# Kernel tuning notes

Hardware: AMD Instinct MI355X
Metric: run time of the kernel (lower is better)

## Reference

```python
import jax, jax.numpy as jnp
import numpy as np

N_NODES = 100000
N_EDGES = 3200000
N_FEAT = 128
HIDDEN = 16
MLP_H = 100
N_CLASSES = 12
N_GRAPHS = 512


def setup_inputs() -> dict:
    key = jax.random.key(0)
    ks = jax.random.split(key, 12)
    x = jax.random.normal(ks[0], (N_NODES, N_FEAT), dtype=jnp.float32)
    edge_index = jax.random.randint(ks[1], (2, N_EDGES), 0, N_NODES, dtype=jnp.int64)
    batch_vec = jnp.sort(jax.random.randint(ks[2], (N_NODES,), 0, N_GRAPHS, dtype=jnp.int64))
    def glorot(k, shape):
        lim = np.sqrt(6.0 / (shape[0] + shape[1]))
        return jax.random.uniform(k, shape, jnp.float32, -lim, lim)
    W1 = glorot(ks[3], (N_FEAT, HIDDEN)); b1 = jnp.zeros((HIDDEN,), jnp.float32)
    W2 = glorot(ks[4], (HIDDEN, HIDDEN)); b2 = jnp.zeros((HIDDEN,), jnp.float32)
    lw1 = glorot(ks[5], (HIDDEN, MLP_H)); lb1 = jnp.zeros((MLP_H,), jnp.float32)
    lw2 = glorot(ks[6], (MLP_H, N_CLASSES)); lb2 = jnp.zeros((N_CLASSES,), jnp.float32)
    return {"x": x, "edge_index": edge_index, "batch_vec": batch_vec,
            "W1": W1, "b1": b1, "W2": W2, "b2": b2,
            "lw1": lw1, "lb1": lb1, "lw2": lw2, "lb2": lb2}


def _gcn_edges(edge_index):
    # add self loops, compute symmetric normalization (PyG GCNConv default)
    loop = jnp.arange(N_NODES, dtype=edge_index.dtype)
    src = jnp.concatenate([edge_index[0], loop])
    dst = jnp.concatenate([edge_index[1], loop])
    deg = jax.ops.segment_sum(jnp.ones_like(dst, dtype=jnp.float32), dst,
                              num_segments=N_NODES)
    dinv = jnp.where(deg > 0, jax.lax.rsqrt(deg), 0.0)
    norm = dinv[src] * dinv[dst]  # [E+N]
    return src, dst, norm


def _gcn_conv(x, W, b, src, dst, norm):
    h = x @ W                                # [N, out]
    msg = h[src] * norm[:, None]             # gather + scale, [E+N, out]
    out = jax.ops.segment_sum(msg, dst, num_segments=N_NODES)
    return out + b


def reference(x, edge_index, batch_vec, W1, b1, W2, b2, lw1, lb1, lw2, lb2):
    src, dst, norm = _gcn_edges(edge_index)
    h = jax.nn.relu(_gcn_conv(x, W1, b1, src, dst, norm))   # dropout: eval no-op
    h = _gcn_conv(h, W2, b2, src, dst, norm)
    h = jax.nn.relu(h)
    pooled = jax.ops.segment_sum(h, batch_vec, num_segments=N_GRAPHS)  # global_add_pool
    g = jax.nn.relu(pooled)
    g = jax.nn.relu(g @ lw1 + lb1)
    return g @ lw2 + lb2  # [N_GRAPHS, N_CLASSES] logits
```

## Files before the change

### kernel.cpp

```cpp
#include <hip/hip_runtime.h>

#define N_NODES   100000
#define N_EDGES   3200000
#define N_FEAT    128
#define HIDDEN    16
#define MLP_H     100
#define N_CLASSES 12
#define N_GRAPHS  512
#define BNODES    512
#define NBUCK     196
#define BCAP      17328
#define CPAD      16
#define RING      64
#define BIN_BLOCKS 256
#define GEMM_BLOCKS 391

__global__ __launch_bounds__(256) void kInit(int* __restrict__ gcursor,
                                             float* __restrict__ pooled) {
    int t = blockIdx.x * 256 + threadIdx.x;
    if (t < NBUCK) gcursor[t * CPAD] = t * BCAP;
    if (t < N_GRAPHS * HIDDEN) pooled[t] = 0.f;
}

__global__ __launch_bounds__(256) void kBinGemm(const int* __restrict__ src,
                                                const int* __restrict__ dst,
                                                int* __restrict__ gcursor,
                                                int* __restrict__ pairs,
                                                const float* __restrict__ x,
                                                const float* __restrict__ W1,
                                                float* __restrict__ hp) {
    __shared__ union {
        struct { int ring[NBUCK * RING]; int cnt[NBUCK]; int fl[NBUCK]; } bin;
        float gw[N_FEAT * HIDDEN];
    } sm;
    int t = threadIdx.x;
    if (blockIdx.x < BIN_BLOCKS) {
        for (int i = t; i < NBUCK; i += 256) { sm.bin.cnt[i] = 0; sm.bin.fl[i] = 0; }
        __syncthreads();
        const int batch = 256 * 4;
        for (int base = blockIdx.x * batch; base < N_EDGES;
             base += BIN_BLOCKS * batch) {
            int e0 = base + t * 4;
            if (e0 < N_EDGES) {
                int4 d4 = *(const int4*)&dst[e0];
                int4 s4 = *(const int4*)&src[e0];
                int dd[4] = {d4.x, d4.y, d4.z, d4.w};
                int ss[4] = {s4.x, s4.y, s4.z, s4.w};
#pragma unroll
                for (int k = 0; k < 4; ++k) {
                    int b = dd[k] >> 9;
                    int p = atomicAdd(&sm.bin.cnt[b], 1);
                    sm.bin.ring[b * RING + (p & (RING - 1))] =
                        (ss[k] << 9) | (dd[k] & 511);
                }
            }
            __syncthreads();
            if (t < NBUCK) {
                while (sm.bin.cnt[t] - sm.bin.fl[t] >= 16) {
                    int start = sm.bin.fl[t];
                    int gpos = atomicAdd(&gcursor[t * CPAD], 16);
                    int rbase = t * RING + (start & (RING - 1));
                    const int4* rp = (const int4*)&sm.bin.ring[rbase];
                    int4* gp = (int4*)&pairs[gpos];
                    gp[0] = rp[0]; gp[1] = rp[1]; gp[2] = rp[2]; gp[3] = rp[3];
                    sm.bin.fl[t] = start + 16;
                }
            }
            __syncthreads();
        }
        if (t < NBUCK) {
            int pending = sm.bin.cnt[t] - sm.bin.fl[t];
            if (pending > 0) {
                int gpos = atomicAdd(&gcursor[t * CPAD], pending);
                for (int k = 0; k < pending; ++k)
                    pairs[gpos + k] =
                        sm.bin.ring[t * RING + ((sm.bin.fl[t] + k) & (RING - 1))];
            }
        }
    } else {
        for (int i = t; i < N_FEAT * HIDDEN; i += 256) sm.gw[i] = W1[i];
        __syncthreads();
        int n = (blockIdx.x - BIN_BLOCKS) * 256 + t;
        if (n >= N_NODES) return;
        float acc[HIDDEN];
#pragma unroll
        for (int j = 0; j < HIDDEN; ++j) acc[j] = 0.f;
        const float4* xr = (const float4*)(x + (size_t)n * N_FEAT);
#pragma unroll 4
        for (int k4 = 0; k4 < N_FEAT / 4; ++k4) {
            float4 v = xr[k4];
            float xk[4] = {v.x, v.y, v.z, v.w};
#pragma unroll
            for (int kk = 0; kk < 4; ++kk) {
                const float4* wrow = (const float4*)&sm.gw[(k4 * 4 + kk) * HIDDEN];
#pragma unroll
                for (int j4 = 0; j4 < 4; ++j4) {
                    float4 wv = wrow[j4];
                    acc[j4 * 4 + 0] += xk[kk] * wv.x;
                    acc[j4 * 4 + 1] += xk[kk] * wv.y;
                    acc[j4 * 4 + 2] += xk[kk] * wv.z;
                    acc[j4 * 4 + 3] += xk[kk] * wv.w;
                }
            }
        }
        float4* hr = (float4*)(hp + (size_t)n * HIDDEN);
#pragma unroll
        for (int j4 = 0; j4 < 4; ++j4)
            hr[j4] = make_float4(acc[j4 * 4 + 0], acc[j4 * 4 + 1],
                                 acc[j4 * 4 + 2], acc[j4 * 4 + 3]);
    }
}

__global__ __launch_bounds__(512) void kBuild(const int* __restrict__ gcursor,
                                              int* __restrict__ pairs,
                                              int2* __restrict__ odc,
                                              float* __restrict__ hp) {
    __shared__ int lp[BCAP];
    __shared__ int hist[BNODES];
    __shared__ int sc[BNODES];
    __shared__ int lcur[BNODES];
    __shared__ float dvl[BNODES];
    int b = blockIdx.x, t = threadIdx.x;
    int base = b * BCAP;
    int cnt = gcursor[b * CPAD] - base;
    for (int i = t; i < cnt; i += 512) lp[i] = pairs[base + i];
    hist[t] = 0;
    __syncthreads();
    for (int i = t; i < cnt; i += 512) atomicAdd(&hist[lp[i] & 511], 1);
    __syncthreads();
    sc[t] = hist[t];
    __syncthreads();
    for (int s = 1; s < 512; s <<= 1) {
        int a = (t >= s) ? sc[t - s] : 0;
        __syncthreads();
        sc[t] += a;
        __syncthreads();
    }
    int g = b * BNODES + t;
    int excl = base + sc[t] - hist[t];
    lcur[t] = excl;
    dvl[t] = rsqrtf((float)hist[t] + 1.0f);
    if (g < N_NODES) odc[g] = make_int2(excl, hist[t]);
    __syncthreads();
    for (int i = t; i < cnt; i += 512) {
        int v = lp[i];
        int pos = atomicAdd(&lcur[v & 511], 1);
        pairs[pos] = (v >> 9) << 6;
    }
    __syncthreads();
    int fbase = b * BNODES * HIDDEN;
#pragma unroll
    for (int i = 0; i < 16; ++i) {
        int f = i * 512 + t;
        int gi = fbase + f;
        if (gi < N_NODES * HIDDEN) hp[gi] *= dvl[f >> 4];
    }
}

template <int MODE>
__global__ __launch_bounds__(256)
void kAgg(const float* __restrict__ hp, const int2* __restrict__ odc,
          const int* __restrict__ csr, const float* __restrict__ W2,
          const float* __restrict__ bias, float* __restrict__ outbuf,
          const int* __restrict__ batch, float* __restrict__ pooled) {
    __shared__ float W2s[HIDDEN * HIDDEN];
    __shared__ float bs[HIDDEN];
    __shared__ float red[256];
    __shared__ int sseg[2];
    int t = threadIdx.x;
    if (MODE == 1) W2s[t] = W2[t];
    if (t < HIDDEN) bs[t] = bias[t];
    int n0 = blockIdx.x * 16;
    if (MODE == 0) {
        if (t == 0) sseg[0] = batch[n0];
        if (t == 1) sseg[1] = batch[n0 + 15];
    }
    __syncthreads();

    int gid = blockIdx.x * 256 + t;
    int n = gid >> 4;
    int j = gid & 15;
    int2 oc = odc[n];
    int beg = oc.x, deg = oc.y;
    int end = beg + deg;
    const char* hpc = (const char*)hp;
    int jb = j << 2;
    float acc = hp[(size_t)n * HIDDEN + j];
    int pv = (beg + j < end) ? csr[beg + j] : -1;
    for (int cur = beg; cur < end; cur += 16) {
        int nxt = cur + 16;
        int pn = (nxt + j < end) ? csr[nxt + j] : -1;
        int s[16];
#pragma unroll
        for (int k = 0; k < 16; ++k) s[k] = __shfl(pv, k, 16);
        float f[16];
#pragma unroll
        for (int k = 0; k < 16; ++k)
            f[k] = (s[k] >= 0) ? *(const float*)(hpc + s[k] + jb) : 0.f;
#pragma unroll
        for (int k = 0; k < 16; ++k) acc += f[k];
        pv = pn;
    }
    float dv = rsqrtf((float)deg + 1.0f);
    if (MODE == 1) {
        float tt = fmaxf(acc * dv + bs[j], 0.f);
        float o = 0.f;
#pragma unroll
        for (int k = 0; k < 16; ++k)
            o += __shfl(tt, k, 16) * W2s[k * HIDDEN + j];
        outbuf[(size_t)n * HIDDEN + j] = o * dv;
    } else {
        float val = fmaxf(acc * dv + bs[j], 0.f);
        int ln = t >> 4;
        red[t] = val;
        __syncthreads();
        if (sseg[0] == sseg[1]) {
            if (ln < 8) red[t] += red[t + 128];
            __syncthreads();
            if (ln < 4) red[t] += red[t + 64];
            __syncthreads();
            if (ln < 2) red[t] += red[t + 32];
            __syncthreads();
            if (ln == 0)
                unsafeAtomicAdd(&pooled[(size_t)sseg[0] * HIDDEN + j],
                                red[t] + red[t + 16]);
        } else {
            unsafeAtomicAdd(&pooled[(size_t)batch[n] * HIDDEN + j], val);
        }
    }
}

__global__ __launch_bounds__(64) void kMlp(const float* __restrict__ pooled,
                                           const float* __restrict__ lw1,
                                           const float* __restrict__ lb1,
                                           const float* __restrict__ lw2,
                                           const float* __restrict__ lb2,
                                           float* __restrict__ out) {
    int g = blockIdx.x * 64 + threadIdx.x;
    if (g >= N_GRAPHS) return;
    float gv[HIDDEN];
#pragma unroll
    for (int k = 0; k < HIDDEN; ++k)
        gv[k] = fmaxf(pooled[(size_t)g * HIDDEN + k], 0.f);
    float o[N_CLASSES];
#pragma unroll
    for (int c = 0; c < N_CLASSES; ++c) o[c] = lb2[c];
    for (int j = 0; j < MLP_H; ++j) {
        float s = lb1[j];
#pragma unroll
        for (int k = 0; k < HIDDEN; ++k) s += gv[k] * lw1[k * MLP_H + j];
        s = fmaxf(s, 0.f);
#pragma unroll
        for (int c = 0; c < N_CLASSES; ++c) o[c] += s * lw2[j * N_CLASSES + c];
    }
#pragma unroll
    for (int c = 0; c < N_CLASSES; ++c) out[(size_t)g * N_CLASSES + c] = o[c];
}

extern "C" void kernel_launch(void* const* d_in, const int* in_sizes, int n_in,
                              void* d_out, int out_size, void* d_ws,
                              size_t ws_size, hipStream_t stream) {
    const float* x     = (const float*)d_in[0];
    const int*   ei    = (const int*)d_in[1];
    const int*   batch = (const int*)d_in[2];
    const float* W1    = (const float*)d_in[3];
    const float* b1    = (const float*)d_in[4];
    const float* W2    = (const float*)d_in[5];
    const float* b2    = (const float*)d_in[6];
    const float* lw1   = (const float*)d_in[7];
    const float* lb1   = (const float*)d_in[8];
    const float* lw2   = (const float*)d_in[9];
    const float* lb2   = (const float*)d_in[10];
    float* out = (float*)d_out;

    const int* src = ei;
    const int* dst = ei + N_EDGES;

    char*  ws      = (char*)d_ws;
    int*   gcursor = (int*)(ws + 0);
    int2*  odc     = (int2*)(ws + 16384);
    int*   pairs   = (int*)(ws + 816384);
    float* hp      = (float*)(ws + 14401536);
    float* hp2     = (float*)(ws + 20801536);
    float* pooled  = (float*)(ws + 27201536);

    kInit<<<32, 256, 0, stream>>>(gcursor, pooled);
    kBinGemm<<<BIN_BLOCKS + GEMM_BLOCKS, 256, 0, stream>>>(
        src, dst, gcursor, pairs, x, W1, hp);
    kBuild<<<NBUCK, 512, 0, stream>>>(gcursor, pairs, odc, hp);
    kAgg<1><<<N_NODES / 16, 256, 0, stream>>>(hp, odc, pairs, W2, b1, hp2,
                                              nullptr, nullptr);
    kAgg<0><<<N_NODES / 16, 256, 0, stream>>>(hp2, odc, pairs, nullptr, b2,
                                              nullptr, batch, pooled);
    kMlp<<<(N_GRAPHS + 63) / 64, 64, 0, stream>>>(pooled, lw1, lb1, lw2, lb2, out);
}
```

Baseline: 166.3 us.

## Vectorize CSR gather to float4 per lane and use nontemporal streaming loads

```diff
diff --git a/kernel.cpp b/kernel.cpp
--- a/kernel.cpp
+++ b/kernel.cpp
@@ -15,6 +15,9 @@
 #define BIN_BLOCKS 256
 #define GEMM_BLOCKS 391
 
+typedef int   vint4  __attribute__((ext_vector_type(4)));
+typedef float vfloat4 __attribute__((ext_vector_type(4)));
+
 __global__ __launch_bounds__(256) void kInit(int* __restrict__ gcursor,
                                              float* __restrict__ pooled) {
     int t = blockIdx.x * 256 + threadIdx.x;
@@ -42,8 +45,8 @@
              base += BIN_BLOCKS * batch) {
             int e0 = base + t * 4;
             if (e0 < N_EDGES) {
-                int4 d4 = *(const int4*)&dst[e0];
-                int4 s4 = *(const int4*)&src[e0];
+                vint4 d4 = __builtin_nontemporal_load((const vint4*)&dst[e0]);
+                vint4 s4 = __builtin_nontemporal_load((const vint4*)&src[e0]);
                 int dd[4] = {d4.x, d4.y, d4.z, d4.w};
                 int ss[4] = {s4.x, s4.y, s4.z, s4.w};
 #pragma unroll
@@ -85,10 +88,10 @@
         float acc[HIDDEN];
 #pragma unroll
         for (int j = 0; j < HIDDEN; ++j) acc[j] = 0.f;
-        const float4* xr = (const float4*)(x + (size_t)n * N_FEAT);
+        const vfloat4* xr = (const vfloat4*)(x + (size_t)n * N_FEAT);
 #pragma unroll 4
         for (int k4 = 0; k4 < N_FEAT / 4; ++k4) {
-            float4 v = xr[k4];
+            vfloat4 v = __builtin_nontemporal_load(&xr[k4]);
             float xk[4] = {v.x, v.y, v.z, v.w};
 #pragma unroll
             for (int kk = 0; kk < 4; ++kk) {
@@ -179,38 +182,61 @@
 
     int gid = blockIdx.x * 256 + t;
     int n = gid >> 4;
-    int j = gid & 15;
+    int l16 = gid & 15;
+    int jj = l16 & 3;
+    int eq = l16 >> 2;
     int2 oc = odc[n];
     int beg = oc.x, deg = oc.y;
     int end = beg + deg;
     const char* hpc = (const char*)hp;
-    int jb = j << 2;
-    float acc = hp[(size_t)n * HIDDEN + j];
-    int pv = (beg + j < end) ? csr[beg + j] : -1;
-    for (int cur = beg; cur < end; cur += 16) {
-        int nxt = cur + 16;
-        int pn = (nxt + j < end) ? csr[nxt + j] : -1;
-        int s[16];
-#pragma unroll
-        for (int k = 0; k < 16; ++k) s[k] = __shfl(pv, k, 16);
-        float f[16];
-#pragma unroll
-        for (int k = 0; k < 16; ++k)
-            f[k] = (s[k] >= 0) ? *(const float*)(hpc + s[k] + jb) : 0.f;
-#pragma unroll
-        for (int k = 0; k < 16; ++k) acc += f[k];
-        pv = pn;
-    }
+    int jb = jj << 4;
+    float4 a4 = make_float4(0.f, 0.f, 0.f, 0.f);
+
+    int pv0 = (beg + l16 < end)      ? csr[beg + l16]      : -1;
+    int pv1 = (beg + 16 + l16 < end) ? csr[beg + 16 + l16] : -1;
+    for (int cur = beg; cur < end; cur += 32) {
+        int nxt = cur + 32;
+        int pn0 = (nxt + l16 < end)      ? csr[nxt + l16]      : -1;
+        int pn1 = (nxt + 16 + l16 < end) ? csr[nxt + 16 + l16] : -1;
+        int sb[8];
+#pragma unroll
+        for (int k = 0; k < 4; ++k) {
+            sb[k]     = __shfl(pv0, k * 4 + eq, 16);
+            sb[4 + k] = __shfl(pv1, k * 4 + eq, 16);
+        }
+        float4 v[8];
+#pragma unroll
+        for (int q = 0; q < 8; ++q)
+            v[q] = (sb[q] >= 0) ? *(const float4*)(hpc + sb[q] + jb)
+                                : make_float4(0.f, 0.f, 0.f, 0.f);
+#pragma unroll
+        for (int q = 0; q < 8; ++q) {
+            a4.x += v[q].x; a4.y += v[q].y; a4.z += v[q].z; a4.w += v[q].w;
+        }
+        pv0 = pn0; pv1 = pn1;
+    }
+    a4.x += __shfl_xor(a4.x, 4, 16);  a4.y += __shfl_xor(a4.y, 4, 16);
+    a4.z += __shfl_xor(a4.z, 4, 16);  a4.w += __shfl_xor(a4.w, 4, 16);
+    a4.x += __shfl_xor(a4.x, 8, 16);  a4.y += __shfl_xor(a4.y, 8, 16);
+    a4.z += __shfl_xor(a4.z, 8, 16);  a4.w += __shfl_xor(a4.w, 8, 16);
+    int srcl = l16 >> 2;
+    float c0 = __shfl(a4.x, srcl, 16);
+    float c1 = __shfl(a4.y, srcl, 16);
+    float c2 = __shfl(a4.z, srcl, 16);
+    float c3 = __shfl(a4.w, srcl, 16);
+    int cc = l16 & 3;
+    float acc = (cc == 0) ? c0 : (cc == 1) ? c1 : (cc == 2) ? c2 : c3;
+    acc += hp[(size_t)n * HIDDEN + l16];
     float dv = rsqrtf((float)deg + 1.0f);
     if (MODE == 1) {
-        float tt = fmaxf(acc * dv + bs[j], 0.f);
+        float tt = fmaxf(acc * dv + bs[l16], 0.f);
         float o = 0.f;
 #pragma unroll
         for (int k = 0; k < 16; ++k)
-            o += __shfl(tt, k, 16) * W2s[k * HIDDEN + j];
-        outbuf[(size_t)n * HIDDEN + j] = o * dv;
+            o += __shfl(tt, k, 16) * W2s[k * HIDDEN + l16];
+        outbuf[(size_t)n * HIDDEN + l16] = o * dv;
     } else {
-        float val = fmaxf(acc * dv + bs[j], 0.f);
+        float val = fmaxf(acc * dv + bs[l16], 0.f);
         int ln = t >> 4;
         red[t] = val;
         __syncthreads();
@@ -222,10 +248,10 @@
             if (ln < 2) red[t] += red[t + 32];
             __syncthreads();
             if (ln == 0)
-                unsafeAtomicAdd(&pooled[(size_t)sseg[0] * HIDDEN + j],
+                unsafeAtomicAdd(&pooled[(size_t)sseg[0] * HIDDEN + l16],
                                 red[t] + red[t + 16]);
         } else {
-            unsafeAtomicAdd(&pooled[(size_t)batch[n] * HIDDEN + j], val);
+            unsafeAtomicAdd(&pooled[(size_t)batch[n] * HIDDEN + l16], val);
         }
     }
 }
```

Measured after the change: 188.2 us. 13.1% more time.
